# Kernel tuning notes

Hardware: AMD Instinct MI355X
Metric: run time of the kernel (lower is better)

The kernel has to match this reference:

```python
import jax, jax.numpy as jnp
import numpy as np

IN_CH = 1024   # backbone channels
N_T = 81       # n_targets (COCO classes + bg)
K = 7          # PSROI grid size
H = 100        # feature map height
WID = 100      # feature map width
R = 1024       # number of regions
S = 2          # bilinear sampling points per bin edge (PSROIAlign-style average)


def setup_inputs() -> dict:
    key = jax.random.key(0)
    k1, k2, k3 = jax.random.split(key, 3)
    x = jax.random.normal(k1, (IN_CH, H, WID), dtype=jnp.float32)
    # regions: fractional (i, j, h, w) = (center_y, center_x, height, width) in [0,1]
    regions = jax.random.uniform(k2, (R, 4), dtype=jnp.float32)
    conv_w = jax.random.normal(k3, (N_T * K * K, IN_CH), dtype=jnp.float32) * 0.02
    conv_b = jnp.zeros((N_T * K * K,), dtype=jnp.float32)
    return {"x": x, "regions": regions, "conv_w": conv_w, "conv_b": conv_b}


def _bilinear_pool(map_thw, ys, xs):
    """Average of bilinear samples of one bin's score map.

    map_thw: (T, H, W) score map for this (u, v) bin's channel group.
    ys: (R, S) sample row coords.  xs: (R, S) sample col coords.
    Returns (R, T): per-region average-pooled bin value.
    """
    Hm, Wm = map_thw.shape[1], map_thw.shape[2]
    ys = jnp.clip(ys, 0.0, Hm - 1)
    xs = jnp.clip(xs, 0.0, Wm - 1)
    y0 = jnp.floor(ys)
    x0 = jnp.floor(xs)
    y0i = y0.astype(jnp.int32)
    x0i = x0.astype(jnp.int32)
    y1i = jnp.minimum(y0i + 1, Hm - 1)
    x1i = jnp.minimum(x0i + 1, Wm - 1)
    wy1 = ys - y0
    wy0 = 1.0 - wy1
    wx1 = xs - x0
    wx0 = 1.0 - wx1

    def g(yi, xi):  # gather (T, R, S, S)
        return map_thw[:, yi[:, :, None], xi[:, None, :]]

    v = (g(y0i, x0i) * (wy0[:, :, None] * wx0[:, None, :])
         + g(y0i, x1i) * (wy0[:, :, None] * wx1[:, None, :])
         + g(y1i, x0i) * (wy1[:, :, None] * wx0[:, None, :])
         + g(y1i, x1i) * (wy1[:, :, None] * wx1[:, None, :]))
    return v.mean((2, 3)).T  # (R, T)


def reference(x, regions, conv_w, conv_b):
    # 1x1 conv score map: (n_targets*k^2, H, W)
    sm = jnp.einsum('oc,chw->ohw', conv_w, x) + conv_b[:, None, None]
    sm = sm.reshape(N_T, K, K, H, WID)  # (T, ky, kx, H, W) position-sensitive groups

    # region geometry (fractional center/size -> absolute feature-map coords)
    top = (regions[:, 0] - regions[:, 2] * 0.5) * H     # (R,)
    left = (regions[:, 1] - regions[:, 3] * 0.5) * WID  # (R,)
    bh = regions[:, 2] * H / K                          # bin height
    bw = regions[:, 3] * WID / K                        # bin width

    off = (jnp.arange(S, dtype=jnp.float32) + 0.5) / S  # (S,) sample offsets in bin
    bins = jnp.arange(K, dtype=jnp.float32)             # (K,)
    ys = top[:, None, None] + (bins[None, :, None] + off[None, None, :]) * bh[:, None, None]   # (R,K,S)
    xs = left[:, None, None] + (bins[None, :, None] + off[None, None, :]) * bw[:, None, None]  # (R,K,S)

    # vmap over the k x k position-sensitive bins; bin (u,v) reads channel group (:,u,v)
    inner = jax.vmap(_bilinear_pool, in_axes=(1, None, 1))  # over kx: sm axis, xs axis
    outer = jax.vmap(inner, in_axes=(1, 1, None))           # over ky: sm axis, ys axis
    pooled = outer(sm, ys, xs)  # (K, K, R, T)

    # pooled.mean(-1).mean(-1) over the k x k grid
    scores = pooled.mean((0, 1))  # (R, T)
    return scores
```

## Files before the change

### kernel.cpp

```cpp
#include <hip/hip_runtime.h>
#include <cstddef>

#define IN_CH 1024
#define NT    81
#define KGRID 7
#define NBINS 49
#define HH    100
#define WW    100
#define NPIX  (HH*WW)
#define NREG  1024
#define COLB  82
#define NCOL  (NBINS*COLB)
#define NPADW 4096
#define SMSTR NCOL

typedef unsigned short ushortT;
typedef short bf16x8 __attribute__((ext_vector_type(8)));
typedef float f32x4  __attribute__((ext_vector_type(4)));

static __device__ __forceinline__ unsigned short f2bf(float f) {
    unsigned int u = __builtin_bit_cast(unsigned int, f);
    return (unsigned short)((u + 0x7fffu + ((u >> 16) & 1u)) >> 16);
}

static __device__ __forceinline__ void gld_lds16(const ushortT* g, ushortT* l) {
    __builtin_amdgcn_global_load_lds(
        (__attribute__((address_space(1))) void*)(unsigned long long)(uintptr_t)g,
        (__attribute__((address_space(3))) void*)(unsigned int)(unsigned long long)(uintptr_t)l,
        16, 0, 0);
}

__global__ __launch_bounds__(256) void prep_x(const float* __restrict__ x,
                                              ushortT* __restrict__ xbT) {
    __shared__ float tile[64][33];
    const int tid = threadIdx.x;
    const int p0 = blockIdx.x * 64;
    const int c0 = blockIdx.y * 32;
    const int pl = tid & 63;
    const int cg = tid >> 6;
#pragma unroll
    for (int cc = 0; cc < 8; ++cc) {
        const int c = cg * 8 + cc;
        const int p = p0 + pl;
        tile[pl][c] = (p < NPIX) ? x[(size_t)(c0 + c) * NPIX + p] : 0.0f;
    }
    __syncthreads();
#pragma unroll
    for (int ph = 0; ph < 4; ++ph) {
        const int plr = ph * 16 + (tid >> 4);
        const int p = p0 + plr;
        const int c = (tid & 15) * 2;
        if (p < NPIX) {
            const unsigned int pk = (unsigned int)f2bf(tile[plr][c]) |
                                    ((unsigned int)f2bf(tile[plr][c + 1]) << 16);
            *(unsigned int*)(xbT + (size_t)p * IN_CH + c0 + c) = pk;
        }
    }
}

__global__ __launch_bounds__(256) void prep_w(const float* __restrict__ conv_w,
                                              ushortT* __restrict__ Wr) {
    const int row = blockIdx.x;
    const int bin = row / COLB;
    const int t   = row - bin * COLB;
    const int c   = threadIdx.x * 4;
    uint2 pk; pk.x = 0; pk.y = 0;
    if (bin < NBINS && t < NT) {
        const float4 v = *(const float4*)(conv_w + ((size_t)(t * NBINS + bin)) * IN_CH + c);
        pk.x = (unsigned int)f2bf(v.x) | ((unsigned int)f2bf(v.y) << 16);
        pk.y = (unsigned int)f2bf(v.z) | ((unsigned int)f2bf(v.w) << 16);
    }
    *(uint2*)(Wr + (size_t)row * IN_CH + c) = pk;
}

__global__ __launch_bounds__(256) void gemm_sm(const ushortT* __restrict__ xbT,
                                               const ushortT* __restrict__ Wr,
                                               ushortT* __restrict__ sm) {
    __shared__ ushortT a_lds[128 * 32];
    __shared__ ushortT b_lds[128 * 32];
    const int tid  = threadIdx.x;
    const int lane = tid & 63;
    const int w    = tid >> 6;
    const int wm   = w & 1;
    const int wn   = w >> 1;
    const int n0   = blockIdx.x * 128;
    const int p0   = blockIdx.y * 128;

    const int srow0 = w * 32 + (lane >> 2);
    const int scol  = (lane & 3) * 8;
    int ap0 = p0 + srow0;      if (ap0 > NPIX - 1) ap0 = NPIX - 1;
    int ap1 = p0 + srow0 + 16; if (ap1 > NPIX - 1) ap1 = NPIX - 1;
    const ushortT* ag0 = xbT + (size_t)ap0 * IN_CH + scol;
    const ushortT* ag1 = xbT + (size_t)ap1 * IN_CH + scol;
    const ushortT* bg0 = Wr + (size_t)(n0 + srow0) * IN_CH + scol;
    const ushortT* bg1 = Wr + (size_t)(n0 + srow0 + 16) * IN_CH + scol;
    ushortT* al0 = a_lds + (w * 32) * 32;
    ushortT* al1 = a_lds + (w * 32 + 16) * 32;
    ushortT* bl0 = b_lds + (w * 32) * 32;
    ushortT* bl1 = b_lds + (w * 32 + 16) * 32;

    const int m_lane = lane & 15;
    const int k0     = (lane >> 4) * 8;

    f32x4 acc[4][4];
#pragma unroll
    for (int mt = 0; mt < 4; ++mt)
#pragma unroll
        for (int nt = 0; nt < 4; ++nt) acc[mt][nt] = (f32x4){0.f, 0.f, 0.f, 0.f};

    for (int kc = 0; kc < IN_CH / 32; ++kc) {
        __syncthreads();
        gld_lds16(ag0, al0);
        gld_lds16(ag1, al1);
        gld_lds16(bg0, bl0);
        gld_lds16(bg1, bl1);
        ag0 += 32; ag1 += 32; bg0 += 32; bg1 += 32;
        __syncthreads();

        bf16x8 af[4], bf[4];
#pragma unroll
        for (int mt = 0; mt < 4; ++mt)
            af[mt] = *(const bf16x8*)(a_lds + (wm * 64 + mt * 16 + m_lane) * 32 + k0);
#pragma unroll
        for (int nt = 0; nt < 4; ++nt)
            bf[nt] = *(const bf16x8*)(b_lds + (wn * 64 + nt * 16 + m_lane) * 32 + k0);
#pragma unroll
        for (int mt = 0; mt < 4; ++mt)
#pragma unroll
            for (int nt = 0; nt < 4; ++nt)
                acc[mt][nt] = __builtin_amdgcn_mfma_f32_16x16x32_bf16(af[mt], bf[nt], acc[mt][nt], 0, 0, 0);
    }

    const int prow_base = p0 + wm * 64 + (lane >> 4) * 4;
    const int ncol_base = n0 + wn * 64 + m_lane;
#pragma unroll
    for (int mt = 0; mt < 4; ++mt) {
#pragma unroll
        for (int rg = 0; rg < 4; ++rg) {
            const int p = prow_base + mt * 16 + rg;
            if (p < NPIX) {
#pragma unroll
                for (int nt = 0; nt < 4; ++nt) {
                    const int n = ncol_base + nt * 16;
                    if (n < NCOL) sm[(size_t)p * SMSTR + n] = f2bf(acc[mt][nt][rg]);
                }
            }
        }
    }
}

__global__ __launch_bounds__(256) void pool_kernel(const ushortT* __restrict__ sm,
                                                   const float* __restrict__ regions,
                                                   const float* __restrict__ conv_b,
                                                   float* __restrict__ out) {
    __shared__ int   pofs[784];
    __shared__ float pw[784];
    __shared__ int   rowo[28]; __shared__ float roww[28];
    __shared__ int   coli[28]; __shared__ float colw[28];
    __shared__ float part[4][COLB];
    const int tid = threadIdx.x;
    const int r = blockIdx.x;

    if (tid < 28) {
        const float4 reg = *(const float4*)(regions + (size_t)r * 4);
        const float top = (reg.x - reg.z * 0.5f) * (float)HH;
        const float bh  = reg.z * ((float)HH / (float)KGRID);
        const int u = tid >> 2, i = tid & 3;
        const int s = i >> 1, hi = i & 1;
        float y = top + ((float)u + ((float)s + 0.5f) * 0.5f) * bh;
        y = fminf(fmaxf(y, 0.0f), (float)(HH - 1));
        const float y0f = floorf(y);
        const int y0 = (int)y0f;
        const float wy1 = y - y0f;
        rowo[tid] = (hi ? min(y0 + 1, HH - 1) : y0) * WW;
        roww[tid] = hi ? wy1 : (1.0f - wy1);
    } else if (tid >= 32 && tid < 60) {
        const float4 reg = *(const float4*)(regions + (size_t)r * 4);
        const float left = (reg.y - reg.w * 0.5f) * (float)WW;
        const float bw   = reg.w * ((float)WW / (float)KGRID);
        const int idx = tid - 32;
        const int v = idx >> 2, j = idx & 3;
        const int s = j >> 1, hi = j & 1;
        float xx = left + ((float)v + ((float)s + 0.5f) * 0.5f) * bw;
        xx = fminf(fmaxf(xx, 0.0f), (float)(WW - 1));
        const float x0f = floorf(xx);
        const int x0 = (int)x0f;
        const float wx1 = xx - x0f;
        coli[idx] = hi ? min(x0 + 1, WW - 1) : x0;
        colw[idx] = hi ? wx1 : (1.0f - wx1);
    }
    __syncthreads();
    for (int tt = tid; tt < 784; tt += 256) {
        const int bin = tt >> 4, tap = tt & 15;
        const int u = bin / KGRID, v = bin - u * KGRID;
        const int i = tap >> 2, j = tap & 3;
        const int pix = rowo[u * 4 + i] + coli[v * 4 + j];
        pofs[tt] = pix * SMSTR + bin * COLB;
        pw[tt]   = roww[u * 4 + i] * colw[v * 4 + j] * (1.0f / 196.0f);
    }
    __syncthreads();
    const int lane = tid & 63, w = tid >> 6;
    if (lane < COLB / 2) {
        float accx = 0.f, accy = 0.f;
        const int l2 = lane * 2;
#pragma unroll 4
        for (int tt = w; tt < 784; tt += 4) {
            const unsigned int v = *(const unsigned int*)(sm + pofs[tt] + l2);
            const float wt = pw[tt];
            accx += wt * __builtin_bit_cast(float, v << 16);
            accy += wt * __builtin_bit_cast(float, v & 0xffff0000u);
        }
        part[w][l2] = accx; part[w][l2 + 1] = accy;
    }
    __syncthreads();
    if (tid < NT) {
        const float sv = part[0][tid] + part[1][tid] + part[2][tid] + part[3][tid];
        float b = 0.f;
        for (int bin = 0; bin < NBINS; ++bin) b += conv_b[tid * NBINS + bin];
        out[(size_t)r * NT + tid] = sv + b * (1.0f / (float)NBINS);
    }
}

__global__ __launch_bounds__(256) void xpose_kernel(const float* __restrict__ x,
                                                    float* __restrict__ xt) {
    __shared__ float tile[32][33];
    const int p0 = blockIdx.x * 32;
    const int c0 = blockIdx.y * 32;
    const int tx = threadIdx.x;
    const int ty = threadIdx.y;
#pragma unroll
    for (int k = 0; k < 32; k += 8) {
        const int p = p0 + tx;
        if (p < NPIX) tile[ty + k][tx] = x[(size_t)(c0 + ty + k) * NPIX + p];
    }
    __syncthreads();
#pragma unroll
    for (int k = 0; k < 32; k += 8) {
        const int p = p0 + ty + k;
        if (p < NPIX) xt[(size_t)p * IN_CH + (c0 + tx)] = tile[tx][ty + k];
    }
}

template <bool XPOSED>
__global__ __launch_bounds__(256) void psroi_kernel(
    const float* __restrict__ xsrc, const float* __restrict__ regions,
    const float* __restrict__ conv_w, const float* __restrict__ conv_b,
    float* __restrict__ out) {
    __shared__ float w_lds[32 * 96];
    __shared__ float g_lds[32 * 64];
    __shared__ int   rowoff[64][4];
    __shared__ float rowwf[64][4];
    __shared__ int   colidx[64][4];
    __shared__ float colwf[64][4];
    const int tid = threadIdx.x;
    const int bin = blockIdx.x >> 4;
    const int rg  = blockIdx.x & 15;
    const int u = bin / KGRID, v = bin % KGRID;
    const int r0 = rg * 64;
    if (tid < 64) {
        const float4 reg = *(const float4*)(regions + (size_t)(r0 + tid) * 4);
        const float top  = (reg.x - reg.z * 0.5f) * (float)HH;
        const float left = (reg.y - reg.w * 0.5f) * (float)WW;
        const float bh = reg.z * ((float)HH / (float)KGRID);
        const float bw = reg.w * ((float)WW / (float)KGRID);
        const float scale = 1.0f / 196.0f;
#pragma unroll
        for (int s = 0; s < 2; s++) {
            const float off = (s + 0.5f) * 0.5f;
            float yy = top + ((float)u + off) * bh;
            yy = fminf(fmaxf(yy, 0.0f), (float)(HH - 1));
            const float y0f = floorf(yy);
            const int y0 = (int)y0f;
            const float wy1 = yy - y0f;
            rowoff[tid][2 * s] = y0 * WW;
            rowoff[tid][2 * s + 1] = min(y0 + 1, HH - 1) * WW;
            rowwf[tid][2 * s] = (1.0f - wy1) * scale;
            rowwf[tid][2 * s + 1] = wy1 * scale;
            float xx = left + ((float)v + off) * bw;
            xx = fminf(fmaxf(xx, 0.0f), (float)(WW - 1));
            const float x0f = floorf(xx);
            const int x0 = (int)x0f;
            const float wx1 = xx - x0f;
            colidx[tid][2 * s] = x0;
            colidx[tid][2 * s + 1] = min(x0 + 1, WW - 1);
            colwf[tid][2 * s] = 1.0f - wx1;
            colwf[tid][2 * s + 1] = wx1;
        }
    }
    const int ri = tid & 15, tq = tid >> 4, rb = tid >> 2, cq = tid & 3;
    float acc[4][6];
#pragma unroll
    for (int m = 0; m < 4; m++)
#pragma unroll
        for (int k = 0; k < 6; k++) acc[m][k] = 0.0f;
    for (int chunk = 0; chunk < IN_CH / 32; chunk++) {
        const int c0 = chunk * 32;
        __syncthreads();
#pragma unroll
        for (int it = 0; it < 12; it++) {
            const int idx = it * 256 + tid;
            const int t = idx >> 5, c = idx & 31;
            float val = 0.0f;
            if (t < NT) val = conv_w[(size_t)(t * NBINS + bin) * IN_CH + c0 + c];
            w_lds[c * 96 + t] = val;
        }
        const int cbase = c0 + cq * 8;
        float g8[8];
#pragma unroll
        for (int cc = 0; cc < 8; cc++) g8[cc] = 0.0f;
#pragma unroll
        for (int i = 0; i < 4; i++) {
            const int ro = rowoff[rb][i];
            const float wy = rowwf[rb][i];
#pragma unroll
            for (int j = 0; j < 4; j++) {
                const int pix = ro + colidx[rb][j];
                const float wv = wy * colwf[rb][j];
                if (XPOSED) {
                    const float4* p = (const float4*)(xsrc + (size_t)pix * IN_CH + cbase);
                    const float4 a = p[0]; const float4 b = p[1];
                    g8[0] += wv * a.x; g8[1] += wv * a.y; g8[2] += wv * a.z; g8[3] += wv * a.w;
                    g8[4] += wv * b.x; g8[5] += wv * b.y; g8[6] += wv * b.z; g8[7] += wv * b.w;
                } else {
#pragma unroll
                    for (int cc = 0; cc < 8; cc++)
                        g8[cc] += wv * xsrc[(size_t)(cbase + cc) * NPIX + pix];
                }
            }
        }
#pragma unroll
        for (int cc = 0; cc < 8; cc++) g_lds[(cq * 8 + cc) * 64 + rb] = g8[cc];
        __syncthreads();
#pragma unroll 4
        for (int c = 0; c < 32; c++) {
            float wv[6];
#pragma unroll
            for (int k = 0; k < 6; k++) wv[k] = w_lds[c * 96 + tq * 6 + k];
            const float4 gq = *(const float4*)&g_lds[c * 64 + ri * 4];
            const float gm[4] = {gq.x, gq.y, gq.z, gq.w};
#pragma unroll
            for (int m = 0; m < 4; m++)
#pragma unroll
                for (int k = 0; k < 6; k++) acc[m][k] += gm[m] * wv[k];
        }
    }
    const float invK2 = 1.0f / 49.0f;
#pragma unroll
    for (int k = 0; k < 6; k++) {
        const int t = tq * 6 + k;
        if (t < NT) {
            const float bterm = conv_b[t * NBINS + bin] * invK2;
#pragma unroll
            for (int m = 0; m < 4; m++) {
                const int rr = r0 + ri * 4 + m;
                atomicAdd(&out[(size_t)rr * NT + t], acc[m][k] + bterm);
            }
        }
    }
}

extern "C" void kernel_launch(void* const* d_in, const int* in_sizes, int n_in,
                              void* d_out, int out_size, void* d_ws, size_t ws_size,
                              hipStream_t stream) {
    const float* x       = (const float*)d_in[0];
    const float* regions = (const float*)d_in[1];
    const float* conv_w  = (const float*)d_in[2];
    const float* conv_b  = (const float*)d_in[3];
    float* out = (float*)d_out;

    const size_t sz_xbT = (size_t)NPIX * IN_CH * 2;
    const size_t sz_Wr  = (size_t)NPADW * IN_CH * 2;
    const size_t sz_sm  = (size_t)NPIX * SMSTR * 2;
    const size_t need   = sz_xbT + sz_Wr + sz_sm;

    if (ws_size >= need) {
        ushortT* xbT = (ushortT*)d_ws;
        ushortT* Wr  = (ushortT*)((char*)d_ws + sz_xbT);
        ushortT* sm  = (ushortT*)((char*)d_ws + sz_xbT + sz_Wr);
        prep_x<<<dim3((NPIX + 63) / 64, IN_CH / 32), 256, 0, stream>>>(x, xbT);
        prep_w<<<dim3(NPADW), 256, 0, stream>>>(conv_w, Wr);
        gemm_sm<<<dim3(NPADW / 128, (NPIX + 127) / 128), 256, 0, stream>>>(xbT, Wr, sm);
        pool_kernel<<<dim3(NREG), 256, 0, stream>>>(sm, regions, conv_b, out);
    } else {
        hipMemsetAsync(out, 0, (size_t)out_size * sizeof(float), stream);
        const size_t xt_bytes = (size_t)NPIX * IN_CH * sizeof(float);
        const dim3 mainGrid(NBINS * 16);
        if (ws_size >= xt_bytes) {
            float* xt = (float*)d_ws;
            xpose_kernel<<<dim3((NPIX + 31) / 32, IN_CH / 32), dim3(32, 8), 0, stream>>>(x, xt);
            psroi_kernel<true><<<mainGrid, 256, 0, stream>>>(xt, regions, conv_w, conv_b, out);
        } else {
            psroi_kernel<false><<<mainGrid, 256, 0, stream>>>(x, regions, conv_w, conv_b, out);
        }
    }
}
```

Baseline: 242.0 us.

## Split pool kernel across 8 tap groups per region with atomic accumulation

The pooling kernel now launches 8 blocks per region, each handling 98 of the 784 bilinear taps, and combines partial sums with atomicAdd into a zeroed output. The per-bin column block is padded from 82 to 84 so each lane can issue an 8-byte load covering four bf16 values, with 12 partial-sum slots per block. This raises parallelism and memory-level concurrency in the gather-bound pooling stage. In exchange it adds a memset, atomics, and redundant geometry setup per block, and the padded score map makes the GEMM and its output slightly larger.

Result: slower. 252.0 us (+4.1%).

```diff
diff --git a/kernel.cpp b/kernel.cpp
--- a/kernel.cpp
+++ b/kernel.cpp
@@ -9,10 +9,11 @@
 #define WW    100
 #define NPIX  (HH*WW)
 #define NREG  1024
-#define COLB  82
+#define COLB  84
 #define NCOL  (NBINS*COLB)
-#define NPADW 4096
+#define NPADW 4224
 #define SMSTR NCOL
+#define NG    8
 
 typedef unsigned short ushortT;
 typedef short bf16x8 __attribute__((ext_vector_type(8)));
@@ -21,6 +22,12 @@
 static __device__ __forceinline__ unsigned short f2bf(float f) {
     unsigned int u = __builtin_bit_cast(unsigned int, f);
     return (unsigned short)((u + 0x7fffu + ((u >> 16) & 1u)) >> 16);
+}
+static __device__ __forceinline__ float bf_lo(unsigned int v) {
+    return __builtin_bit_cast(float, v << 16);
+}
+static __device__ __forceinline__ float bf_hi(unsigned int v) {
+    return __builtin_bit_cast(float, v & 0xffff0000u);
 }
 
 static __device__ __forceinline__ void gld_lds16(const ushortT* g, ushortT* l) {
@@ -153,13 +160,14 @@
                                                    const float* __restrict__ regions,
                                                    const float* __restrict__ conv_b,
                                                    float* __restrict__ out) {
-    __shared__ int   pofs[784];
-    __shared__ float pw[784];
     __shared__ int   rowo[28]; __shared__ float roww[28];
     __shared__ int   coli[28]; __shared__ float colw[28];
-    __shared__ float part[4][COLB];
+    __shared__ int   pofs_l[98];
+    __shared__ float pw_l[98];
+    __shared__ float part[12][84];
     const int tid = threadIdx.x;
     const int r = blockIdx.x;
+    const int g = blockIdx.y;
 
     if (tid < 28) {
         const float4 reg = *(const float4*)(regions + (size_t)r * 4);
@@ -190,34 +198,46 @@
         colw[idx] = hi ? wx1 : (1.0f - wx1);
     }
     __syncthreads();
-    for (int tt = tid; tt < 784; tt += 256) {
+    if (tid < 98) {
+        const int tt = g * 98 + tid;
         const int bin = tt >> 4, tap = tt & 15;
         const int u = bin / KGRID, v = bin - u * KGRID;
         const int i = tap >> 2, j = tap & 3;
         const int pix = rowo[u * 4 + i] + coli[v * 4 + j];
-        pofs[tt] = pix * SMSTR + bin * COLB;
-        pw[tt]   = roww[u * 4 + i] * colw[v * 4 + j] * (1.0f / 196.0f);
+        pofs_l[tid] = pix * SMSTR + bin * COLB;
+        pw_l[tid]   = roww[u * 4 + i] * colw[v * 4 + j] * (1.0f / 196.0f);
     }
     __syncthreads();
+
     const int lane = tid & 63, w = tid >> 6;
-    if (lane < COLB / 2) {
-        float accx = 0.f, accy = 0.f;
-        const int l2 = lane * 2;
-#pragma unroll 4
-        for (int tt = w; tt < 784; tt += 4) {
-            const unsigned int v = *(const unsigned int*)(sm + pofs[tt] + l2);
-            const float wt = pw[tt];
-            accx += wt * __builtin_bit_cast(float, v << 16);
-            accy += wt * __builtin_bit_cast(float, v & 0xffff0000u);
-        }
-        part[w][l2] = accx; part[w][l2 + 1] = accy;
+    const int sub  = lane / 21;
+    const int cidx = lane - sub * 21;
+    float a0 = 0.f, a1 = 0.f, a2 = 0.f, a3 = 0.f;
+    if (sub < 3) {
+#pragma unroll
+        for (int it = 0; it < 9; ++it) {
+            const int lt = it * 12 + w * 3 + sub;
+            if (lt < 98) {
+                const uint2 v = *(const uint2*)(sm + pofs_l[lt] + cidx * 4);
+                const float wt = pw_l[lt];
+                a0 += wt * bf_lo(v.x); a1 += wt * bf_hi(v.x);
+                a2 += wt * bf_lo(v.y); a3 += wt * bf_hi(v.y);
+            }
+        }
+        float4 p4; p4.x = a0; p4.y = a1; p4.z = a2; p4.w = a3;
+        *(float4*)&part[w * 3 + sub][cidx * 4] = p4;
     }
     __syncthreads();
     if (tid < NT) {
-        const float sv = part[0][tid] + part[1][tid] + part[2][tid] + part[3][tid];
-        float b = 0.f;
-        for (int bin = 0; bin < NBINS; ++bin) b += conv_b[tid * NBINS + bin];
-        out[(size_t)r * NT + tid] = sv + b * (1.0f / (float)NBINS);
+        float v = 0.f;
+#pragma unroll
+        for (int s = 0; s < 12; ++s) v += part[s][tid];
+        if (g == 0) {
+            float b = 0.f;
+            for (int bin = 0; bin < NBINS; ++bin) b += conv_b[tid * NBINS + bin];
+            v += b * (1.0f / (float)NBINS);
+        }
+        atomicAdd(out + (size_t)r * NT + tid, v);
     }
 }
 
@@ -377,10 +397,11 @@
         ushortT* xbT = (ushortT*)d_ws;
         ushortT* Wr  = (ushortT*)((char*)d_ws + sz_xbT);
         ushortT* sm  = (ushortT*)((char*)d_ws + sz_xbT + sz_Wr);
+        hipMemsetAsync(out, 0, (size_t)out_size * sizeof(float), stream);
         prep_x<<<dim3((NPIX + 63) / 64, IN_CH / 32), 256, 0, stream>>>(x, xbT);
         prep_w<<<dim3(NPADW), 256, 0, stream>>>(conv_w, Wr);
         gemm_sm<<<dim3(NPADW / 128, (NPIX + 127) / 128), 256, 0, stream>>>(xbT, Wr, sm);
-        pool_kernel<<<dim3(NREG), 256, 0, stream>>>(sm, regions, conv_b, out);
+        pool_kernel<<<dim3(NREG, NG), 256, 0, stream>>>(sm, regions, conv_b, out);
     } else {
         hipMemsetAsync(out, 0, (size_t)out_size * sizeof(float), stream);
         const size_t xt_bytes = (size_t)NPIX * IN_CH * sizeof(float);
```
